# Performance work log

Measured on AMD Instinct MI355X. Metric: run time of the kernel, lower is better.

The kernel has to match this reference:

```python
import jax, jax.numpy as jnp
from jax import lax
import numpy as np

H = 32  # hidden_size


def setup_inputs() -> dict:
    key = jax.random.key(0)
    ks = jax.random.split(key, 12)
    B, T, I = 4096, 1024, 1
    s = lambda fan_in: 1.0 / np.sqrt(fan_in)
    inp = {
        "x": jax.random.normal(ks[0], (B, I, T), dtype=jnp.float32),
        # LSTM params, PyTorch layout: gates stacked as [i, f, g, o]
        "W_ih": jax.random.uniform(ks[1], (4 * H, I), jnp.float32, -s(H), s(H)),
        "W_hh": jax.random.uniform(ks[2], (4 * H, H), jnp.float32, -s(H), s(H)),
        "b_ih": jax.random.uniform(ks[3], (4 * H,), jnp.float32, -s(H), s(H)),
        "b_hh": jax.random.uniform(ks[4], (4 * H,), jnp.float32, -s(H), s(H)),
        # MLP head: 32 -> 16 -> 8 -> 1
        "W1": jax.random.uniform(ks[5], (16, H), jnp.float32, -s(H), s(H)),
        "b1": jax.random.uniform(ks[6], (16,), jnp.float32, -s(H), s(H)),
        "W2": jax.random.uniform(ks[7], (8, 16), jnp.float32, -s(16), s(16)),
        "b2": jax.random.uniform(ks[8], (8,), jnp.float32, -s(16), s(16)),
        "W3": jax.random.uniform(ks[9], (1, 8), jnp.float32, -s(8), s(8)),
        "b3": jax.random.uniform(ks[10], (1,), jnp.float32, -s(8), s(8)),
    }
    return inp


def reference(x, W_ih, W_hh, b_ih, b_hh, W1, b1, W2, b2, W3, b3):
    # x: (B, 1, T) -> (B, T, 1), batch_first LSTM over T
    xs = jnp.transpose(x, (0, 2, 1))
    B, T, _ = xs.shape
    # Precompute input contribution to all gates: (B, T, 4H)
    xW = jnp.einsum('bti,gi->btg', xs, W_ih) + (b_ih + b_hh)

    def step(carry, xw_t):
        h, c = carry
        gates = xw_t + h @ W_hh.T  # (B, 4H)
        i, f, g, o = jnp.split(gates, 4, axis=-1)
        c = jax.nn.sigmoid(f) * c + jax.nn.sigmoid(i) * jnp.tanh(g)
        h = jax.nn.sigmoid(o) * jnp.tanh(c)
        return (h, c), None

    h0 = jnp.zeros((B, H), xs.dtype)
    (h_n, _), _ = lax.scan(step, (h0, h0), jnp.swapaxes(xW, 0, 1))

    # MLP head on final hidden state h_n[-1] (single layer -> h_n itself)
    out = jax.nn.relu(h_n @ W1.T + b1)
    out = jax.nn.relu(out @ W2.T + b2)
    return out @ W3.T + b3  # (B, 1)
```

## Files before the change

kernel.cpp:

```cpp
#include <hip/hip_runtime.h>

#define HSZ 32
#define TT  1024
#define LOG2E 1.44269504088896340736f

typedef float v2f __attribute__((ext_vector_type(2)));
typedef float v4f __attribute__((ext_vector_type(4)));

__device__ __forceinline__ float frcp(float x)  { return __builtin_amdgcn_rcpf(x); }
__device__ __forceinline__ float fexp2(float x) { return __builtin_amdgcn_exp2f(x); }

__global__ __launch_bounds__(64, 4)
void lstm_fused_kernel(const float* __restrict__ x,
                       const float* __restrict__ W_ih,
                       const float* __restrict__ W_hh,
                       const float* __restrict__ b_ih,
                       const float* __restrict__ b_hh,
                       const float* __restrict__ W1, const float* __restrict__ b1,
                       const float* __restrict__ W2, const float* __restrict__ b2,
                       const float* __restrict__ W3, const float* __restrict__ b3,
                       float* __restrict__ out)
{
  __shared__ __align__(16) float hlds[2][HSZ];

  const int lane = threadIdx.x;
  const int half = lane >> 5;
  const int j    = lane & 31;
  const int elem = blockIdx.x;

  const int r1 = (half ? 2 : 0) * HSZ + j;
  const int r2 = (half ? 3 : 1) * HSZ + j;
  const float s1 = half ? (-2.0f * LOG2E) : (-LOG2E);
  const float s2 = -LOG2E;
  const float A1 = half ? 2.0f : 1.0f;
  const float B1 = half ? -1.0f : 0.0f;

  v2f w1[16], w2[16];
  {
    const v4f* p1 = reinterpret_cast<const v4f*>(W_hh + r1 * HSZ);
    const v4f* p2 = reinterpret_cast<const v4f*>(W_hh + r2 * HSZ);
#pragma unroll
    for (int k4 = 0; k4 < 8; ++k4) {
      v4f a = p1[k4] * s1;
      v4f b = p2[k4] * s2;
      w1[2*k4] = a.lo; w1[2*k4+1] = a.hi;
      w2[2*k4] = b.lo; w2[2*k4+1] = b.hi;
    }
  }
  const float bz1  = s1 * (b_ih[r1] + b_hh[r1]);
  const float bz2  = s2 * (b_ih[r2] + b_hh[r2]);
  const float wxz1 = s1 * W_ih[r1];
  const float wxz2 = s2 * W_ih[r2];

  v2f h2[16];
#pragma unroll
  for (int k = 0; k < 16; ++k) h2[k] = (v2f){0.0f, 0.0f};
  float c = 0.0f;

  const float* xrow = x + (size_t)elem * TT;

#pragma unroll 1
  for (int t0 = 0; t0 < TT; t0 += 64) {
    float xc = xrow[t0 + lane];

#pragma unroll
    for (int k = 0; k < 16; k += 4) {
      asm volatile("" : "+v"(w1[k]), "+v"(w1[k+1]), "+v"(w1[k+2]), "+v"(w1[k+3]),
                        "+v"(w2[k]), "+v"(w2[k+1]), "+v"(w2[k+2]), "+v"(w2[k+3]));
    }

#pragma unroll 1
    for (int s = 0; s < 64; ++s) {
      float xt = __shfl(xc, s);

      v2f a1 = (v2f){bz1, 0.0f};
      v2f a2 = (v2f){bz2, 0.0f};
#pragma unroll
      for (int k = 0; k < 16; ++k) {
        a1 = __builtin_elementwise_fma(w1[k], h2[k], a1);
        a2 = __builtin_elementwise_fma(w2[k], h2[k], a2);
      }
      float z1 = a1.x + fmaf(xt, wxz1, a1.y);
      float z2 = a2.x + fmaf(xt, wxz2, a2.y);

      float act1 = fmaf(A1, frcp(1.0f + fexp2(z1)), B1);
      float act2 = frcp(1.0f + fexp2(z2));

      float tg = __shfl_xor(act1, 32);
      float so = __shfl_xor(act2, 32);

      c = fmaf(act2, c, act1 * tg);
      float tc = fmaf(2.0f, frcp(1.0f + fexp2(c * (-2.0f * LOG2E))), -1.0f);
      float h = so * tc;

      hlds[half][j] = h;
#pragma unroll
      for (int k4 = 0; k4 < 8; ++k4) {
        v4f v = *reinterpret_cast<const v4f*>(&hlds[0][4 * k4]);
        h2[2*k4]   = v.lo;
        h2[2*k4+1] = v.hi;
      }
    }
  }

  const float* hrow = &hlds[0][0];
  float a1v[16];
#pragma unroll
  for (int r = 0; r < 16; ++r) {
    float acc = b1[r];
#pragma unroll
    for (int k = 0; k < 32; ++k) acc = fmaf(W1[r * 32 + k], hrow[k], acc);
    a1v[r] = fmaxf(acc, 0.0f);
  }
  float a2v[8];
#pragma unroll
  for (int r = 0; r < 8; ++r) {
    float acc = b2[r];
#pragma unroll
    for (int k = 0; k < 16; ++k) acc = fmaf(W2[r * 16 + k], a1v[k], acc);
    a2v[r] = fmaxf(acc, 0.0f);
  }
  float o = b3[0];
#pragma unroll
  for (int k = 0; k < 8; ++k) o = fmaf(W3[k], a2v[k], o);

  if (lane == 0) out[elem] = o;
}

extern "C" void kernel_launch(void* const* d_in, const int* in_sizes, int n_in,
                              void* d_out, int out_size, void* d_ws, size_t ws_size,
                              hipStream_t stream) {
  const float* x    = (const float*)d_in[0];
  const float* W_ih = (const float*)d_in[1];
  const float* W_hh = (const float*)d_in[2];
  const float* b_ih = (const float*)d_in[3];
  const float* b_hh = (const float*)d_in[4];
  const float* W1   = (const float*)d_in[5];
  const float* b1   = (const float*)d_in[6];
  const float* W2   = (const float*)d_in[7];
  const float* b2   = (const float*)d_in[8];
  const float* W3   = (const float*)d_in[9];
  const float* b3   = (const float*)d_in[10];
  float* out = (float*)d_out;

  const int B = in_sizes[0] / TT;
  dim3 grid(B), block(64);
  hipLaunchKernelGGL(lstm_fused_kernel, grid, block, 0, stream,
                     x, W_ih, W_hh, b_ih, b_hh, W1, b1, W2, b2, W3, b3, out);
}
```

Baseline: 580.6 us.

## Use fp16 packed dot products for recurrent matvec with preconverted weights

Converts the scaled W_hh rows to packed fp16 pairs in a small prep kernel that writes to workspace, and the main kernel loads them with inline asm dwordx4 loads. The recurrent matvec now uses v_dot2 (fp16 inputs, fp32 accumulate) reading h directly from LDS stored as fp16, which halves register footprint and the LDS traffic per step. This trades accuracy, since h and weights are rounded to fp16 across 1024 recurrent steps, and removes the explicit h register copy and the asm register pinning. It also adds an extra kernel launch.

Measured after the change: 499.5 us. -14.0%, faster.

```diff
diff --git a/kernel.cpp b/kernel.cpp
--- a/kernel.cpp
+++ b/kernel.cpp
@@ -4,58 +4,99 @@
 #define TT  1024
 #define LOG2E 1.44269504088896340736f
 
-typedef float v2f __attribute__((ext_vector_type(2)));
-typedef float v4f __attribute__((ext_vector_type(4)));
+typedef _Float16     h2  __attribute__((ext_vector_type(2)));
+typedef float        v4f __attribute__((ext_vector_type(4)));
+typedef unsigned int v4u __attribute__((ext_vector_type(4)));
 
 __device__ __forceinline__ float frcp(float x)  { return __builtin_amdgcn_rcpf(x); }
 __device__ __forceinline__ float fexp2(float x) { return __builtin_amdgcn_exp2f(x); }
+__device__ __forceinline__ h2    bch2(unsigned int u) { return __builtin_bit_cast(h2, u); }
+__device__ __forceinline__ float fdot2(h2 a, h2 b, float c) {
+  return __builtin_amdgcn_fdot2(a, b, c, false);
+}
+
+__global__ void lstm_prep_kernel(const float* __restrict__ W_ih,
+                                 const float* __restrict__ W_hh,
+                                 const float* __restrict__ b_ih,
+                                 const float* __restrict__ b_hh,
+                                 unsigned int* __restrict__ ws)
+{
+  const int lane = threadIdx.x;
+  const int half = lane >> 5;
+  const int j    = lane & 31;
+  const int r1 = (half ? 2 : 0) * HSZ + j;
+  const int r2 = (half ? 3 : 1) * HSZ + j;
+  const float s1 = half ? (-2.0f * LOG2E) : (-LOG2E);
+  const float s2 = -LOG2E;
+  unsigned int* base = ws + lane * 36;
+  union { h2 h; unsigned int u; } cv;
+  for (int d = 0; d < 16; ++d) {
+    cv.h = (h2){ (_Float16)(s1 * W_hh[r1 * HSZ + 2*d]),
+                 (_Float16)(s1 * W_hh[r1 * HSZ + 2*d + 1]) };
+    base[d] = cv.u;
+    cv.h = (h2){ (_Float16)(s2 * W_hh[r2 * HSZ + 2*d]),
+                 (_Float16)(s2 * W_hh[r2 * HSZ + 2*d + 1]) };
+    base[16 + d] = cv.u;
+  }
+  union { float f; unsigned int u; } fu;
+  fu.f = s1 * (b_ih[r1] + b_hh[r1]); base[32] = fu.u;
+  fu.f = s2 * (b_ih[r2] + b_hh[r2]); base[33] = fu.u;
+  fu.f = s1 * W_ih[r1];              base[34] = fu.u;
+  fu.f = s2 * W_ih[r2];              base[35] = fu.u;
+}
 
 __global__ __launch_bounds__(64, 4)
-void lstm_fused_kernel(const float* __restrict__ x,
-                       const float* __restrict__ W_ih,
-                       const float* __restrict__ W_hh,
-                       const float* __restrict__ b_ih,
-                       const float* __restrict__ b_hh,
+void lstm_fused_kernel(const unsigned int* __restrict__ ws,
+                       const float* __restrict__ x,
                        const float* __restrict__ W1, const float* __restrict__ b1,
                        const float* __restrict__ W2, const float* __restrict__ b2,
                        const float* __restrict__ W3, const float* __restrict__ b3,
                        float* __restrict__ out)
 {
-  __shared__ __align__(16) float hlds[2][HSZ];
+  __shared__ __align__(16) _Float16 hlds[2][HSZ];
 
   const int lane = threadIdx.x;
   const int half = lane >> 5;
   const int j    = lane & 31;
   const int elem = blockIdx.x;
 
-  const int r1 = (half ? 2 : 0) * HSZ + j;
-  const int r2 = (half ? 3 : 1) * HSZ + j;
-  const float s1 = half ? (-2.0f * LOG2E) : (-LOG2E);
-  const float s2 = -LOG2E;
   const float A1 = half ? 2.0f : 1.0f;
   const float B1 = half ? -1.0f : 0.0f;
 
-  v2f w1[16], w2[16];
-  {
-    const v4f* p1 = reinterpret_cast<const v4f*>(W_hh + r1 * HSZ);
-    const v4f* p2 = reinterpret_cast<const v4f*>(W_hh + r2 * HSZ);
+  const unsigned int* wbase = ws + (size_t)lane * 36;
+  v4u wq[8]; v4f cvec;
+  asm volatile(
+    "global_load_dwordx4 %0, %9, off\n\t"
+    "global_load_dwordx4 %1, %9, off offset:16\n\t"
+    "global_load_dwordx4 %2, %9, off offset:32\n\t"
+    "global_load_dwordx4 %3, %9, off offset:48\n\t"
+    "global_load_dwordx4 %4, %9, off offset:64\n\t"
+    "global_load_dwordx4 %5, %9, off offset:80\n\t"
+    "global_load_dwordx4 %6, %9, off offset:96\n\t"
+    "global_load_dwordx4 %7, %9, off offset:112\n\t"
+    "global_load_dwordx4 %8, %9, off offset:128\n\t"
+    "s_waitcnt vmcnt(0)"
+    : "=&v"(wq[0]), "=&v"(wq[1]), "=&v"(wq[2]), "=&v"(wq[3]),
+      "=&v"(wq[4]), "=&v"(wq[5]), "=&v"(wq[6]), "=&v"(wq[7]),
+      "=&v"(cvec)
+    : "v"(wbase)
+    : "memory");
+
+  h2 w1h[16], w2h[16];
 #pragma unroll
-    for (int k4 = 0; k4 < 8; ++k4) {
-      v4f a = p1[k4] * s1;
-      v4f b = p2[k4] * s2;
-      w1[2*k4] = a.lo; w1[2*k4+1] = a.hi;
-      w2[2*k4] = b.lo; w2[2*k4+1] = b.hi;
-    }
+  for (int q = 0; q < 4; ++q) {
+    w1h[4*q+0] = bch2(wq[q].x);   w1h[4*q+1] = bch2(wq[q].y);
+    w1h[4*q+2] = bch2(wq[q].z);   w1h[4*q+3] = bch2(wq[q].w);
+    w2h[4*q+0] = bch2(wq[4+q].x); w2h[4*q+1] = bch2(wq[4+q].y);
+    w2h[4*q+2] = bch2(wq[4+q].z); w2h[4*q+3] = bch2(wq[4+q].w);
   }
-  const float bz1  = s1 * (b_ih[r1] + b_hh[r1]);
-  const float bz2  = s2 * (b_ih[r2] + b_hh[r2]);
-  const float wxz1 = s1 * W_ih[r1];
-  const float wxz2 = s2 * W_ih[r2];
+  const float bz1  = cvec.x;
+  const float bz2  = cvec.y;
+  const float wxz1 = cvec.z;
+  const float wxz2 = cvec.w;
 
-  v2f h2[16];
-#pragma unroll
-  for (int k = 0; k < 16; ++k) h2[k] = (v2f){0.0f, 0.0f};
   float c = 0.0f;
+  hlds[half][j] = (_Float16)0.0f;
 
   const float* xrow = x + (size_t)elem * TT;
 
@@ -63,28 +104,30 @@
   for (int t0 = 0; t0 < TT; t0 += 64) {
     float xc = xrow[t0 + lane];
 
-#pragma unroll
-    for (int k = 0; k < 16; k += 4) {
-      asm volatile("" : "+v"(w1[k]), "+v"(w1[k+1]), "+v"(w1[k+2]), "+v"(w1[k+3]),
-                        "+v"(w2[k]), "+v"(w2[k+1]), "+v"(w2[k+2]), "+v"(w2[k+3]));
-    }
-
 #pragma unroll 1
     for (int s = 0; s < 64; ++s) {
       float xt = __shfl(xc, s);
 
-      v2f a1 = (v2f){bz1, 0.0f};
-      v2f a2 = (v2f){bz2, 0.0f};
+      float a1 = fmaf(xt, wxz1, bz1);
+      float a2 = fmaf(xt, wxz2, bz2);
+
+      const v4u* hv = reinterpret_cast<const v4u*>(&hlds[0][0]);
 #pragma unroll
-      for (int k = 0; k < 16; ++k) {
-        a1 = __builtin_elementwise_fma(w1[k], h2[k], a1);
-        a2 = __builtin_elementwise_fma(w2[k], h2[k], a2);
+      for (int g = 0; g < 4; ++g) {
+        v4u hq = hv[g];
+        h2 p0 = bch2(hq.x), p1 = bch2(hq.y), p2 = bch2(hq.z), p3 = bch2(hq.w);
+        a1 = fdot2(w1h[4*g+0], p0, a1);
+        a2 = fdot2(w2h[4*g+0], p0, a2);
+        a1 = fdot2(w1h[4*g+1], p1, a1);
+        a2 = fdot2(w2h[4*g+1], p1, a2);
+        a1 = fdot2(w1h[4*g+2], p2, a1);
+        a2 = fdot2(w2h[4*g+2], p2, a2);
+        a1 = fdot2(w1h[4*g+3], p3, a1);
+        a2 = fdot2(w2h[4*g+3], p3, a2);
       }
-      float z1 = a1.x + fmaf(xt, wxz1, a1.y);
-      float z2 = a2.x + fmaf(xt, wxz2, a2.y);
 
-      float act1 = fmaf(A1, frcp(1.0f + fexp2(z1)), B1);
-      float act2 = frcp(1.0f + fexp2(z2));
+      float act1 = fmaf(A1, frcp(1.0f + fexp2(a1)), B1);
+      float act2 = frcp(1.0f + fexp2(a2));
 
       float tg = __shfl_xor(act1, 32);
       float so = __shfl_xor(act2, 32);
@@ -93,23 +136,20 @@
       float tc = fmaf(2.0f, frcp(1.0f + fexp2(c * (-2.0f * LOG2E))), -1.0f);
       float h = so * tc;
 
-      hlds[half][j] = h;
-#pragma unroll
-      for (int k4 = 0; k4 < 8; ++k4) {
-        v4f v = *reinterpret_cast<const v4f*>(&hlds[0][4 * k4]);
-        h2[2*k4]   = v.lo;
-        h2[2*k4+1] = v.hi;
-      }
+      hlds[half][j] = (_Float16)h;
     }
   }
 
-  const float* hrow = &hlds[0][0];
+  float hf[HSZ];
+#pragma unroll
+  for (int k = 0; k < HSZ; ++k) hf[k] = (float)hlds[0][k];
+
   float a1v[16];
 #pragma unroll
   for (int r = 0; r < 16; ++r) {
     float acc = b1[r];
 #pragma unroll
-    for (int k = 0; k < 32; ++k) acc = fmaf(W1[r * 32 + k], hrow[k], acc);
+    for (int k = 0; k < 32; ++k) acc = fmaf(W1[r * 32 + k], hf[k], acc);
     a1v[r] = fmaxf(acc, 0.0f);
   }
   float a2v[8];
@@ -142,9 +182,12 @@
   const float* W3   = (const float*)d_in[9];
   const float* b3   = (const float*)d_in[10];
   float* out = (float*)d_out;
+  unsigned int* ws = (unsigned int*)d_ws;
 
   const int B = in_sizes[0] / TT;
-  dim3 grid(B), block(64);
-  hipLaunchKernelGGL(lstm_fused_kernel, grid, block, 0, stream,
-                     x, W_ih, W_hh, b_ih, b_hh, W1, b1, W2, b2, W3, b3, out);
+
+  hipLaunchKernelGGL(lstm_prep_kernel, dim3(1), dim3(64), 0, stream,
+                     W_ih, W_hh, b_ih, b_hh, ws);
+  hipLaunchKernelGGL(lstm_fused_kernel, dim3(B), dim3(64), 0, stream,
+                     ws, x, W1, b1, W2, b2, W3, b3, out);
 }
```
